# Optimization experiments

Measured on AMD Instinct MI355X. Metric: run time of the kernel, lower is better.

Reference implementation:

```python
import jax, jax.numpy as jnp
import numpy as np

jax.config.update("jax_enable_x64", True)

N_NODES = 100000
E0 = 3_200_000
EN = 3_200_000


def setup_inputs() -> dict:
    key = jax.random.key(0)
    k1, k2 = jax.random.split(key)
    A0 = jax.random.randint(k1, (2, E0), 0, N_NODES, dtype=jnp.int64)
    An = jax.random.randint(k2, (2, EN), 0, N_NODES, dtype=jnp.int64)
    p = jnp.float32(0.1)  # learned scalar parameter
    return {"A0_edge_index": A0, "An_edge_index": An, "ver": 1, "p": p}


def reference(A0_edge_index, An_edge_index, ver, p):
    if ver == 1:
        keep_prob = jax.nn.sigmoid(p)
        e0 = A0_edge_index.shape[1]
        # Bernoulli keep-mask over A0 edges (fixed key for determinism)
        mask = jax.random.bernoulli(jax.random.key(42), keep_prob, (e0,))
        SHIFT = jnp.int64(1) << 32  # pack (src,dst) into one int64 code
        SENT = jnp.iinfo(jnp.int64).max
        a0_codes = A0_edge_index[0] * SHIFT + A0_edge_index[1]
        a0_codes = jnp.where(mask, a0_codes, SENT)  # dropped edges -> sentinel
        an_codes = An_edge_index[0] * SHIFT + An_edge_index[1]
        codes = jnp.concatenate([a0_codes, an_codes])
        # sort-based dedup; fixed output size, padded with sentinel
        uniq = jnp.unique(codes, size=codes.shape[0], fill_value=SENT)
        valid = uniq != SENT
        src = jnp.where(valid, uniq // SHIFT, -1)
        dst = jnp.where(valid, uniq % SHIFT, -1)
        return jnp.stack([src, dst])  # [2, E0+EN], padded cols are -1
    else:
        w = jax.nn.sigmoid(p)
        return w * A0_edge_index + (1.0 - w) * An_edge_index
```

## Files before the change

### kernel.cpp

```cpp
#include <hip/hip_runtime.h>
#include <stdint.h>

#define BUK 782
#define CAP 6912
#define CH  8192
#define PAD 16
#define SENTK 0xFFFFFFFFu

__device__ __forceinline__ uint32_t rotl32(uint32_t x, int r) { return (x << r) | (x >> (32 - r)); }

__device__ __forceinline__ uint32_t threefry_bits(uint32_t i) {
  const uint32_t k0 = 0u, k1 = 42u;
  const uint32_t k2 = k0 ^ k1 ^ 0x1BD11BDAu;
  uint32_t x0 = k0;
  uint32_t x1 = i + k1;
#define TF_R(r) { x0 += x1; x1 = rotl32(x1, r); x1 ^= x0; }
  TF_R(13) TF_R(15) TF_R(26) TF_R(6)   x0 += k1; x1 += k2 + 1u;
  TF_R(17) TF_R(29) TF_R(16) TF_R(24)  x0 += k2; x1 += k0 + 2u;
  TF_R(13) TF_R(15) TF_R(26) TF_R(6)   x0 += k0; x1 += k1 + 3u;
  TF_R(17) TF_R(29) TF_R(16) TF_R(24)  x0 += k1; x1 += k2 + 4u;
  TF_R(13) TF_R(15) TF_R(26) TF_R(6)   x0 += k2; x1 += k0 + 5u;
#undef TF_R
  return x0 ^ x1;
}

__device__ __forceinline__ bool keep_edge(uint32_t i, float kp) {
  uint32_t bits = threefry_bits(i);
  float u = __uint_as_float((bits >> 9) | 0x3f800000u) - 1.0f;
  return u < kp;
}

__device__ __forceinline__ float keep_prob(const float* pp) {
  double pd = (double)pp[0];
  return (float)(1.0 / (1.0 + exp(-pd)));
}

__device__ __forceinline__ uint32_t wave_incl_scan(uint32_t v, int lane) {
#pragma unroll
  for (int off = 1; off < 64; off <<= 1) {
    uint32_t t = (uint32_t)__shfl_up((int)v, off, 64);
    if (lane >= off) v += t;
  }
  return v;
}

template <int J>
__device__ __forceinline__ uint32_t xshf(uint32_t v, int lane) {
  if constexpr (J == 1) {
    return (uint32_t)__builtin_amdgcn_mov_dpp((int)v, 0xB1, 0xF, 0xF, true);
  } else if constexpr (J == 2) {
    return (uint32_t)__builtin_amdgcn_mov_dpp((int)v, 0x4E, 0xF, 0xF, true);
  } else if constexpr (J == 4 || J == 8) {
    uint32_t up = (uint32_t)__builtin_amdgcn_mov_dpp((int)v, 0x100 | J, 0xF, 0xF, true);
    uint32_t dn = (uint32_t)__builtin_amdgcn_mov_dpp((int)v, 0x110 | J, 0xF, 0xF, true);
    return (lane & J) ? dn : up;
  } else {
    return (uint32_t)__shfl_xor((int)v, J, 64);
  }
}

__device__ __forceinline__ void cex(uint32_t& v, uint32_t o, bool takeMin) {
  uint32_t mn = v < o ? v : o, mx = v < o ? o : v;
  v = takeMin ? mn : mx;
}
template <int J>
__device__ __forceinline__ void ce1(uint32_t& v, bool takeMin, int lane) {
  cex(v, xshf<J>(v, lane), takeMin);
}

__device__ __forceinline__ uint32_t bitonic64(uint32_t v, int lane) {
#define BS1(J, K) ce1<J>(v, ((lane & (J)) == 0) == ((lane & (K)) == 0), lane)
  BS1(1, 2);
  BS1(2, 4); BS1(1, 4);
  BS1(4, 8); BS1(2, 8); BS1(1, 8);
  BS1(8, 16); BS1(4, 16); BS1(2, 16); BS1(1, 16);
  BS1(16, 32); BS1(8, 32); BS1(4, 32); BS1(2, 32); BS1(1, 32);
  ce1<32>(v, (lane & 32) == 0, lane); ce1<16>(v, (lane & 16) == 0, lane);
  ce1<8>(v, (lane & 8) == 0, lane);   ce1<4>(v, (lane & 4) == 0, lane);
  ce1<2>(v, (lane & 2) == 0, lane);   ce1<1>(v, (lane & 1) == 0, lane);
#undef BS1
  return v;
}

__device__ __forceinline__ void bitonic128(uint32_t& v0, uint32_t& v1, int lane) {
#define BS2(J, K) { bool tm = ((lane & (J)) == 0) == ((lane & (K)) == 0); ce1<J>(v0, tm, lane); ce1<J>(v1, tm, lane); }
  BS2(1, 2);
  BS2(2, 4); BS2(1, 4);
  BS2(4, 8); BS2(2, 8); BS2(1, 8);
  BS2(8, 16); BS2(4, 16); BS2(2, 16); BS2(1, 16);
  BS2(16, 32); BS2(8, 32); BS2(4, 32); BS2(2, 32); BS2(1, 32);
#undef BS2
  ce1<32>(v0, (lane & 32) == 0, lane); ce1<32>(v1, (lane & 32) != 0, lane);
  ce1<16>(v0, (lane & 16) == 0, lane); ce1<16>(v1, (lane & 16) != 0, lane);
  ce1<8>(v0, (lane & 8) == 0, lane);   ce1<8>(v1, (lane & 8) != 0, lane);
  ce1<4>(v0, (lane & 4) == 0, lane);   ce1<4>(v1, (lane & 4) != 0, lane);
  ce1<2>(v0, (lane & 2) == 0, lane);   ce1<2>(v1, (lane & 2) != 0, lane);
  ce1<1>(v0, (lane & 1) == 0, lane);   ce1<1>(v1, (lane & 1) != 0, lane);
  { uint32_t lo = v0 < v1 ? v0 : v1, hi = v0 < v1 ? v1 : v0; v0 = lo; v1 = hi; }
  ce1<32>(v0, (lane & 32) == 0, lane); ce1<32>(v1, (lane & 32) == 0, lane);
  ce1<16>(v0, (lane & 16) == 0, lane); ce1<16>(v1, (lane & 16) == 0, lane);
  ce1<8>(v0, (lane & 8) == 0, lane);   ce1<8>(v1, (lane & 8) == 0, lane);
  ce1<4>(v0, (lane & 4) == 0, lane);   ce1<4>(v1, (lane & 4) == 0, lane);
  ce1<2>(v0, (lane & 2) == 0, lane);   ce1<2>(v1, (lane & 2) == 0, lane);
  ce1<1>(v0, (lane & 1) == 0, lane);   ce1<1>(v1, (lane & 1) == 0, lane);
}

__global__ __launch_bounds__(512) void passA_k(const int* __restrict__ a0,
                                               const int* __restrict__ an,
                                               int e0, int en, const float* __restrict__ pp,
                                               uint32_t* __restrict__ cur_g,
                                               uint32_t* __restrict__ bkt) {
  __shared__ uint32_t stageK[CH];
  __shared__ uint32_t cntA[784];
  __shared__ uint32_t loA[784];
  __shared__ uint32_t gb[784];

  float kp = keep_prob(pp);
  int tid = threadIdx.x;
  int wid = tid >> 6, lane = tid & 63;
  int total = e0 + en;
  int base = blockIdx.x * CH;

  uint32_t key[16];
  uint32_t bkid[16];

  for (int t = tid; t < 784; t += 512) cntA[t] = 0;
  __syncthreads();

#pragma unroll
  for (int k = 0; k < 4; k++) {
    int g = base + 4 * (k * 512 + tid);
    int s4[4], d4[4];
    bool have = false;
    if (g + 3 < e0) {
      int4 sv = *reinterpret_cast<const int4*>(&a0[g]);
      int4 dv = *reinterpret_cast<const int4*>(&a0[e0 + g]);
      s4[0] = sv.x; s4[1] = sv.y; s4[2] = sv.z; s4[3] = sv.w;
      d4[0] = dv.x; d4[1] = dv.y; d4[2] = dv.z; d4[3] = dv.w;
      have = true;
    } else if (g >= e0 && g + 3 < total) {
      int j = g - e0;
      int4 sv = *reinterpret_cast<const int4*>(&an[j]);
      int4 dv = *reinterpret_cast<const int4*>(&an[en + j]);
      s4[0] = sv.x; s4[1] = sv.y; s4[2] = sv.z; s4[3] = sv.w;
      d4[0] = dv.x; d4[1] = dv.y; d4[2] = dv.z; d4[3] = dv.w;
      have = true;
    } else if (g < total) {
      for (int e = 0; e < 4; e++) {
        int idx = g + e;
        if (idx < total) {
          if (idx < e0) { s4[e] = a0[idx]; d4[e] = a0[e0 + idx]; }
          else          { int j = idx - e0; s4[e] = an[j]; d4[e] = an[en + j]; }
        } else { s4[e] = -1; d4[e] = 0; }
      }
      have = true;
    }
#pragma unroll
    for (int e = 0; e < 4; e++) {
      int idx = g + e;
      uint32_t ky = SENTK, b_ = SENTK;
      if (have && idx < total && s4[e] >= 0) {
        bool keep = (idx < e0) ? keep_edge((uint32_t)idx, kp) : true;
        if (keep) {
          uint32_t us = (uint32_t)s4[e];
          b_ = us >> 7;
          if (b_ < BUK) ky = ((us & 127u) << 17) | (uint32_t)d4[e];
          else b_ = SENTK;
        }
      }
      key[k * 4 + e] = ky;
      bkid[k * 4 + e] = b_;
      if (b_ != SENTK) atomicAdd(&cntA[b_], 1u);
    }
  }
  __syncthreads();

  if (wid == 0) {
    uint32_t c[13];
    uint32_t s = 0;
#pragma unroll
    for (int j = 0; j < 13; j++) {
      int idx = lane * 13 + j;
      c[j] = (idx < 784) ? cntA[idx] : 0u;
      s += c[j];
    }
    uint32_t inc = wave_incl_scan(s, lane);
    uint32_t ex = inc - s;
#pragma unroll
    for (int j = 0; j < 13; j++) {
      int idx = lane * 13 + j;
      if (idx < 784) { loA[idx] = ex; gb[idx] = ex; }
      ex += c[j];
    }
  }
  __syncthreads();

#pragma unroll
  for (int k = 0; k < 16; k++) {
    uint32_t b_ = bkid[k];
    if (b_ != SENTK) stageK[atomicAdd(&gb[b_], 1u)] = key[k];
  }
  __syncthreads();

  for (int t = tid; t < BUK; t += 512) {
    uint32_t c = cntA[t];
    if (c) {
      uint32_t gbase = atomicAdd(&cur_g[(size_t)t * PAD], c);
      uint32_t lo = loA[t];
      uint32_t* dstp = bkt + (size_t)t * CAP;
      for (uint32_t j = 0; j < c; j++) {
        uint32_t a = gbase + j;
        if (a < CAP) dstp[a] = stageK[lo + j];
      }
    }
  }
}

__global__ __launch_bounds__(512) void passB_k(uint32_t* __restrict__ bkt,
                                               const uint32_t* __restrict__ cur_g,
                                               uint32_t* __restrict__ ucnt) {
  __shared__ uint32_t lin[CAP];
  __shared__ uint32_t c128[128], lo128[128], cur128[128];
  __shared__ uint32_t u128[128], uo128[128];

  int b = blockIdx.x, tid = threadIdx.x;
  int wid = tid >> 6, lane = tid & 63;
  uint32_t len = cur_g[(size_t)b * PAD];
  if (len > CAP) len = CAP;
  uint32_t* seg = bkt + (size_t)b * CAP;

  if (tid < 128) c128[tid] = 0;
  __syncthreads();

  uint32_t rv[16];
#pragma unroll
  for (int k = 0; k < 4; k++) {
    uint32_t i4 = 4u * (uint32_t)(k * 512 + tid);
    if (i4 + 3 < len) {
      uint4 v = *reinterpret_cast<const uint4*>(&seg[i4]);
      rv[4 * k] = v.x; rv[4 * k + 1] = v.y; rv[4 * k + 2] = v.z; rv[4 * k + 3] = v.w;
    } else {
#pragma unroll
      for (int e = 0; e < 4; e++) rv[4 * k + e] = (i4 + e < len) ? seg[i4 + e] : SENTK;
    }
  }

#pragma unroll
  for (int k = 0; k < 16; k++)
    if (rv[k] != SENTK) atomicAdd(&c128[rv[k] >> 17], 1u);
  __syncthreads();

  if (wid == 0) {
    uint32_t c0 = c128[2 * lane], c1 = c128[2 * lane + 1];
    uint32_t s = c0 + c1;
    uint32_t inc = wave_incl_scan(s, lane);
    uint32_t ex = inc - s;
    lo128[2 * lane] = ex;       lo128[2 * lane + 1] = ex + c0;
    cur128[2 * lane] = ex;      cur128[2 * lane + 1] = ex + c0;
  }
  __syncthreads();

#pragma unroll
  for (int k = 0; k < 16; k++)
    if (rv[k] != SENTK) lin[atomicAdd(&cur128[rv[k] >> 17], 1u)] = rv[k];
  __syncthreads();

  for (int s = wid; s < 128; s += 8) {
    uint32_t L = c128[s], sb = lo128[s];
    if (L > 1u && L <= 64u) {
      uint32_t v = (lane < (int)L) ? lin[sb + lane] : SENTK;
      v = bitonic64(v, lane);
      if (lane < (int)L) lin[sb + lane] = v;
    } else if (L > 64u && L <= 128u) {
      uint32_t v0 = (lane < (int)L) ? lin[sb + lane] : SENTK;
      uint32_t v1 = (64 + lane < (int)L) ? lin[sb + 64 + lane] : SENTK;
      bitonic128(v0, v1, lane);
      if (lane < (int)L) lin[sb + lane] = v0;
      if (64 + lane < (int)L) lin[sb + 64 + lane] = v1;
    } else if (L > 128u) {
      uint32_t* gsc = seg + sb;
      for (uint32_t i0 = lane; i0 < L; i0 += 64) {
        uint32_t x = lin[sb + i0];
        uint32_t pos = 0;
        for (uint32_t j = 0; j < L; j++) {
          uint32_t y = lin[sb + j];
          pos += (y < x || (y == x && j < i0)) ? 1u : 0u;
        }
        gsc[pos] = x;
      }
      asm volatile("s_waitcnt vmcnt(0)" ::: "memory");
      for (uint32_t i0 = lane; i0 < L; i0 += 64) lin[sb + i0] = gsc[i0];
    }
    uint32_t ub = 0;
    for (uint32_t t = 0; t < L; t += 64) {
      uint32_t i = t + lane;
      bool valid = i < L;
      uint32_t x = valid ? lin[sb + i] : 0u;
      uint32_t prev = valid ? lin[sb + (i == 0 ? 0 : i - 1)] : 0u;
      bool uniq = valid && (i == 0 || prev != x);
      unsigned long long ball = __ballot(uniq ? 1 : 0);
      uint32_t rank = (uint32_t)__popcll(ball & ((1ull << lane) - 1ull));
      if (uniq) lin[sb + ub + rank] = x;
      ub += (uint32_t)__popcll(ball);
    }
    if (lane == 0) u128[s] = ub;
  }
  __syncthreads();

  if (wid == 0) {
    uint32_t c0 = u128[2 * lane], c1 = u128[2 * lane + 1];
    uint32_t s = c0 + c1;
    uint32_t inc = wave_incl_scan(s, lane);
    uint32_t ex = inc - s;
    uo128[2 * lane] = ex;       uo128[2 * lane + 1] = ex + c0;
    if (lane == 63) ucnt[b] = inc;
  }
  __syncthreads();

  for (int s = wid; s < 128; s += 8) {
    uint32_t u = u128[s], sb = lo128[s], ob = uo128[s];
    for (uint32_t k2 = lane; k2 < u; k2 += 64) seg[ob + k2] = lin[sb + k2];
  }
}

__global__ __launch_bounds__(64) void uscan_k(const uint32_t* __restrict__ ucnt,
                                              uint32_t* __restrict__ uoff) {
  int lane = threadIdx.x;
  uint32_t c[13];
  uint32_t s = 0;
#pragma unroll
  for (int j = 0; j < 13; j++) {
    int idx = lane * 13 + j;
    c[j] = (idx < BUK) ? ucnt[idx] : 0u;
    s += c[j];
  }
  uint32_t inc = wave_incl_scan(s, lane);
  uint32_t ex = inc - s;
#pragma unroll
  for (int j = 0; j < 13; j++) {
    int idx = lane * 13 + j;
    if (idx < BUK) uoff[idx] = ex;
    ex += c[j];
  }
  if (lane == 63) uoff[BUK] = inc;
}

__global__ __launch_bounds__(256) void passC_k(const uint32_t* __restrict__ bkt,
                                               const uint32_t* __restrict__ uoff,
                                               int* __restrict__ out, int oute) {
  int b = blockIdx.x;
  uint32_t lo = uoff[b], u = uoff[b + 1] - lo;
  const uint32_t* seg = bkt + (size_t)b * CAP;
  for (uint32_t k = threadIdx.x; k < u; k += 256) {
    uint32_t key = seg[k];
    out[lo + k] = (int)((uint32_t)(b << 7) | (key >> 17));
    out[oute + lo + k] = (int)(key & 0x1FFFFu);
  }
}

__global__ void tail_k(const uint32_t* __restrict__ uoff, int* __restrict__ out, int oute) {
  uint32_t total = uoff[BUK];
  for (uint32_t i = blockIdx.x * blockDim.x + threadIdx.x + total; i < (uint32_t)oute;
       i += gridDim.x * blockDim.x) {
    out[i] = -1;
    out[oute + i] = -1;
  }
}

extern "C" void kernel_launch(void* const* d_in, const int* in_sizes, int n_in,
                              void* d_out, int out_size, void* d_ws, size_t ws_size,
                              hipStream_t stream) {
  const int* a0 = (const int*)d_in[0];
  const int* an = (const int*)d_in[1];
  const float* pp = (const float*)d_in[3];
  int e0 = in_sizes[0] / 2;
  int en = in_sizes[1] / 2;
  int M = e0 + en;
  int oute = out_size / 2;

  uint8_t* wbase = (uint8_t*)d_ws;
  size_t o = 0;
  auto nxt = [&](size_t bytes) -> void* {
    void* p = wbase + o;
    o = (o + bytes + 255) & ~(size_t)255;
    return p;
  };
  uint32_t* cur_g = (uint32_t*)nxt((size_t)BUK * PAD * 4);
  uint32_t* ucnt  = (uint32_t*)nxt((size_t)BUK * 4);
  uint32_t* uoff  = (uint32_t*)nxt((size_t)(BUK + 1) * 4);
  uint32_t* bkt   = (uint32_t*)nxt((size_t)BUK * CAP * 4);

  int ablocks = (M + CH - 1) / CH;

  hipMemsetAsync(cur_g, 0, (size_t)BUK * PAD * 4, stream);
  passA_k<<<ablocks, 512, 0, stream>>>(a0, an, e0, en, pp, cur_g, bkt);
  passB_k<<<BUK, 512, 0, stream>>>(bkt, cur_g, ucnt);
  uscan_k<<<1, 64, 0, stream>>>(ucnt, uoff);
  passC_k<<<BUK, 256, 0, stream>>>(bkt, uoff, (int*)d_out, oute);
  tail_k<<<1024, 256, 0, stream>>>(uoff, (int*)d_out, oute);
}
```

Before: 130.7 us.

## Replace global atomic bucket scatter with per-block chunks and offset matrix gather

Pass A now writes each block's locally bucket-sorted keys contiguously into a private chunk with vectorized stores, and records per-bucket offsets in a uint16 matrix, instead of doing global atomicAdd reservations and scattered per-element writes into shared buckets. Pass B gathers each bucket by reading its slice from all 782 chunks via the offset matrix, and uses the output buffer as scratch instead of the bucket array. The final compaction is split into two kernels that copy and then unpack in place inside the output. This removes the global atomics, the memset and the uncoalesced scatter, at the cost of many short strided reads in pass B and an extra kernel launch.

```diff
diff --git a/kernel.cpp b/kernel.cpp
--- a/kernel.cpp
+++ b/kernel.cpp
@@ -2,9 +2,11 @@
 #include <stdint.h>
 
 #define BUK 782
+#define NBLK 782
 #define CAP 6912
 #define CH  8192
-#define PAD 16
+#define LSTR 800
+#define TSTR 8184
 #define SENTK 0xFFFFFFFFu
 
 __device__ __forceinline__ uint32_t rotl32(uint32_t x, int r) { return (x << r) | (x >> (32 - r)); }
@@ -108,12 +110,13 @@
 __global__ __launch_bounds__(512) void passA_k(const int* __restrict__ a0,
                                                const int* __restrict__ an,
                                                int e0, int en, const float* __restrict__ pp,
-                                               uint32_t* __restrict__ cur_g,
-                                               uint32_t* __restrict__ bkt) {
+                                               uint32_t* __restrict__ chunk,
+                                               uint16_t* __restrict__ loAmat) {
   __shared__ uint32_t stageK[CH];
   __shared__ uint32_t cntA[784];
   __shared__ uint32_t loA[784];
   __shared__ uint32_t gb[784];
+  __shared__ uint32_t keptS;
 
   float kp = keep_prob(pp);
   int tid = threadIdx.x;
@@ -192,6 +195,7 @@
       if (idx < 784) { loA[idx] = ex; gb[idx] = ex; }
       ex += c[j];
     }
+    if (lane == 63) keptS = ex;
   }
   __syncthreads();
 
@@ -202,52 +206,52 @@
   }
   __syncthreads();
 
-  for (int t = tid; t < BUK; t += 512) {
-    uint32_t c = cntA[t];
-    if (c) {
-      uint32_t gbase = atomicAdd(&cur_g[(size_t)t * PAD], c);
-      uint32_t lo = loA[t];
-      uint32_t* dstp = bkt + (size_t)t * CAP;
-      for (uint32_t j = 0; j < c; j++) {
-        uint32_t a = gbase + j;
-        if (a < CAP) dstp[a] = stageK[lo + j];
-      }
-    }
-  }
-}
-
-__global__ __launch_bounds__(512) void passB_k(uint32_t* __restrict__ bkt,
-                                               const uint32_t* __restrict__ cur_g,
-                                               uint32_t* __restrict__ ucnt) {
+  uint32_t kept = keptS;
+  uint32_t* dst = chunk + (size_t)blockIdx.x * CH;
+  for (uint32_t i4 = 4u * (uint32_t)tid; i4 + 3 < kept; i4 += 2048u) {
+    uint4 v = make_uint4(stageK[i4], stageK[i4 + 1], stageK[i4 + 2], stageK[i4 + 3]);
+    *reinterpret_cast<uint4*>(&dst[i4]) = v;
+  }
+  if (tid < (int)(kept & 3u)) {
+    uint32_t i = (kept & ~3u) + (uint32_t)tid;
+    dst[i] = stageK[i];
+  }
+  uint16_t* lrow = loAmat + (size_t)blockIdx.x * LSTR;
+  for (int t = tid; t < 785; t += 512) lrow[t] = (uint16_t)((t < 784) ? loA[t] : kept);
+}
+
+__global__ __launch_bounds__(512) void passB_k(const uint32_t* __restrict__ chunk,
+                                               const uint16_t* __restrict__ loAmat,
+                                               uint32_t* __restrict__ ucnt,
+                                               int* __restrict__ out) {
   __shared__ uint32_t lin[CAP];
   __shared__ uint32_t c128[128], lo128[128], cur128[128];
   __shared__ uint32_t u128[128], uo128[128];
 
-  int b = blockIdx.x, tid = threadIdx.x;
+  int k = blockIdx.x, tid = threadIdx.x;
   int wid = tid >> 6, lane = tid & 63;
-  uint32_t len = cur_g[(size_t)b * PAD];
-  if (len > CAP) len = CAP;
-  uint32_t* seg = bkt + (size_t)b * CAP;
 
   if (tid < 128) c128[tid] = 0;
   __syncthreads();
 
-  uint32_t rv[16];
-#pragma unroll
-  for (int k = 0; k < 4; k++) {
-    uint32_t i4 = 4u * (uint32_t)(k * 512 + tid);
-    if (i4 + 3 < len) {
-      uint4 v = *reinterpret_cast<const uint4*>(&seg[i4]);
-      rv[4 * k] = v.x; rv[4 * k + 1] = v.y; rv[4 * k + 2] = v.z; rv[4 * k + 3] = v.w;
-    } else {
-#pragma unroll
-      for (int e = 0; e < 4; e++) rv[4 * k + e] = (i4 + e < len) ? seg[i4 + e] : SENTK;
-    }
-  }
-
-#pragma unroll
-  for (int k = 0; k < 16; k++)
-    if (rv[k] != SENTK) atomicAdd(&c128[rv[k] >> 17], 1u);
+  for (int rb = 0; rb < 2; rb++) {
+    int b = rb * 512 + tid;
+    if (b < NBLK) {
+      uint32_t lo = loAmat[(size_t)b * LSTR + k];
+      uint32_t hi = loAmat[(size_t)b * LSTR + k + 1];
+      const uint32_t* src = chunk + (size_t)b * CH + lo;
+      uint32_t c = hi - lo;
+      uint32_t j = 0;
+      for (; j + 4 <= c; j += 4) {
+        uint32_t v0 = src[j], v1 = src[j + 1], v2 = src[j + 2], v3 = src[j + 3];
+        atomicAdd(&c128[v0 >> 17], 1u);
+        atomicAdd(&c128[v1 >> 17], 1u);
+        atomicAdd(&c128[v2 >> 17], 1u);
+        atomicAdd(&c128[v3 >> 17], 1u);
+      }
+      for (; j < c; j++) atomicAdd(&c128[src[j] >> 17], 1u);
+    }
+  }
   __syncthreads();
 
   if (wid == 0) {
@@ -260,13 +264,25 @@
   }
   __syncthreads();
 
-#pragma unroll
-  for (int k = 0; k < 16; k++)
-    if (rv[k] != SENTK) lin[atomicAdd(&cur128[rv[k] >> 17], 1u)] = rv[k];
+  for (int rb = 0; rb < 2; rb++) {
+    int b = rb * 512 + tid;
+    if (b < NBLK) {
+      uint32_t lo = loAmat[(size_t)b * LSTR + k];
+      uint32_t hi = loAmat[(size_t)b * LSTR + k + 1];
+      const uint32_t* src = chunk + (size_t)b * CH + lo;
+      uint32_t c = hi - lo;
+      for (uint32_t j = 0; j < c; j++) {
+        uint32_t v = src[j];
+        uint32_t p = atomicAdd(&cur128[v >> 17], 1u);
+        if (p < CAP) lin[p] = v;
+      }
+    }
+  }
   __syncthreads();
 
   for (int s = wid; s < 128; s += 8) {
     uint32_t L = c128[s], sb = lo128[s];
+    if (sb + L > CAP) L = (sb < CAP) ? (CAP - sb) : 0;
     if (L > 1u && L <= 64u) {
       uint32_t v = (lane < (int)L) ? lin[sb + lane] : SENTK;
       v = bitonic64(v, lane);
@@ -278,7 +294,7 @@
       if (lane < (int)L) lin[sb + lane] = v0;
       if (64 + lane < (int)L) lin[sb + 64 + lane] = v1;
     } else if (L > 128u) {
-      uint32_t* gsc = seg + sb;
+      uint32_t* gsc = (uint32_t*)out + (size_t)k * TSTR + sb;
       for (uint32_t i0 = lane; i0 < L; i0 += 64) {
         uint32_t x = lin[sb + i0];
         uint32_t pos = 0;
@@ -313,13 +329,14 @@
     uint32_t inc = wave_incl_scan(s, lane);
     uint32_t ex = inc - s;
     uo128[2 * lane] = ex;       uo128[2 * lane + 1] = ex + c0;
-    if (lane == 63) ucnt[b] = inc;
-  }
-  __syncthreads();
-
+    if (lane == 63) ucnt[k] = inc;
+  }
+  __syncthreads();
+
+  int* tdst = out + (size_t)k * TSTR;
   for (int s = wid; s < 128; s += 8) {
     uint32_t u = u128[s], sb = lo128[s], ob = uo128[s];
-    for (uint32_t k2 = lane; k2 < u; k2 += 64) seg[ob + k2] = lin[sb + k2];
+    for (uint32_t k2 = lane; k2 < u; k2 += 64) tdst[ob + k2] = (int)lin[sb + k2];
   }
 }
 
@@ -342,19 +359,25 @@
     if (idx < BUK) uoff[idx] = ex;
     ex += c[j];
   }
-  if (lane == 63) uoff[BUK] = inc;
-}
-
-__global__ __launch_bounds__(256) void passC_k(const uint32_t* __restrict__ bkt,
-                                               const uint32_t* __restrict__ uoff,
-                                               int* __restrict__ out, int oute) {
-  int b = blockIdx.x;
-  uint32_t lo = uoff[b], u = uoff[b + 1] - lo;
-  const uint32_t* seg = bkt + (size_t)b * CAP;
-  for (uint32_t k = threadIdx.x; k < u; k += 256) {
-    uint32_t key = seg[k];
-    out[lo + k] = (int)((uint32_t)(b << 7) | (key >> 17));
-    out[oute + lo + k] = (int)(key & 0x1FFFFu);
+  if (lane == 63) uoff[BUK] = ex;
+}
+
+__global__ __launch_bounds__(256) void passC1_k(const uint32_t* __restrict__ uoff,
+                                                int* __restrict__ out, int oute) {
+  int k = blockIdx.x;
+  uint32_t lo = uoff[k], u = uoff[k + 1] - lo;
+  const int* src = out + (size_t)k * TSTR;
+  for (uint32_t j = threadIdx.x; j < u; j += 256) out[(size_t)oute + lo + j] = src[j];
+}
+
+__global__ __launch_bounds__(256) void passC2_k(const uint32_t* __restrict__ uoff,
+                                                int* __restrict__ out, int oute) {
+  int k = blockIdx.x;
+  uint32_t lo = uoff[k], u = uoff[k + 1] - lo;
+  for (uint32_t j = threadIdx.x; j < u; j += 256) {
+    uint32_t key = (uint32_t)out[(size_t)oute + lo + j];
+    out[lo + j] = (int)(((uint32_t)k << 7) | (key >> 17));
+    out[(size_t)oute + lo + j] = (int)(key & 0x1FFFFu);
   }
 }
 
@@ -385,17 +408,17 @@
     o = (o + bytes + 255) & ~(size_t)255;
     return p;
   };
-  uint32_t* cur_g = (uint32_t*)nxt((size_t)BUK * PAD * 4);
-  uint32_t* ucnt  = (uint32_t*)nxt((size_t)BUK * 4);
-  uint32_t* uoff  = (uint32_t*)nxt((size_t)(BUK + 1) * 4);
-  uint32_t* bkt   = (uint32_t*)nxt((size_t)BUK * CAP * 4);
+  uint32_t* ucnt   = (uint32_t*)nxt((size_t)BUK * 4);
+  uint32_t* uoff   = (uint32_t*)nxt((size_t)(BUK + 1) * 4);
+  uint16_t* loAmat = (uint16_t*)nxt((size_t)NBLK * LSTR * 2);
+  uint32_t* chunk  = (uint32_t*)nxt((size_t)NBLK * CH * 4);
 
   int ablocks = (M + CH - 1) / CH;
 
-  hipMemsetAsync(cur_g, 0, (size_t)BUK * PAD * 4, stream);
-  passA_k<<<ablocks, 512, 0, stream>>>(a0, an, e0, en, pp, cur_g, bkt);
-  passB_k<<<BUK, 512, 0, stream>>>(bkt, cur_g, ucnt);
+  passA_k<<<ablocks, 512, 0, stream>>>(a0, an, e0, en, pp, chunk, loAmat);
+  passB_k<<<BUK, 512, 0, stream>>>(chunk, loAmat, ucnt, (int*)d_out);
   uscan_k<<<1, 64, 0, stream>>>(ucnt, uoff);
-  passC_k<<<BUK, 256, 0, stream>>>(bkt, uoff, (int*)d_out, oute);
+  passC1_k<<<BUK, 256, 0, stream>>>(uoff, (int*)d_out, oute);
+  passC2_k<<<BUK, 256, 0, stream>>>(uoff, (int*)d_out, oute);
   tail_k<<<1024, 256, 0, stream>>>(uoff, (int*)d_out, oute);
 }
```

Result: slower. 156.2 us (+19.5%).
